# Performance work log

Hardware: AMD Instinct MI355X
Metric: run time of the kernel (lower is better)

Reference implementation:

```python
import jax, jax.numpy as jnp
import numpy as np

N_NODES = 20000
N_EDGES = 320000
N_INPUT = 128
N_HIDDEN = 128
N_LAYERS = 3
N_OUT = 2
C_WEIGHT = 1.0
BN_EPS = 1e-5


def _psi(z):
    # sign(z) * log(1 + |z|), the LorentzNet scalar map
    return jnp.sign(z) * jnp.log1p(jnp.abs(z))


def _mink_dot(a, b):
    # Minkowski inner product, metric diag(+1, -1, ..., -1)
    return a[:, 0] * b[:, 0] - jnp.sum(a[:, 1:] * b[:, 1:], axis=1)


def setup_inputs() -> dict:
    key = jax.random.key(0)
    ks = jax.random.split(key, 12)
    n, h, L = N_INPUT, N_HIDDEN, N_LAYERS
    d_in = 2 * n + 6
    f32 = jnp.float32
    inp = {
        "x": jax.random.normal(ks[0], (N_NODES, n), f32),
        "edge_index": jax.random.randint(ks[1], (2, N_EDGES), 0, N_NODES),
        "edge_attr": jax.random.normal(ks[2], (N_EDGES, 4), f32),
        # phi_e: Linear(d_in->h, no bias), BN(h), ReLU, Linear(h->h), ReLU
        "W1": (jax.random.normal(ks[3], (L, d_in, h), f32) / np.sqrt(d_in)).astype(f32),
        "gamma": jnp.ones((L, h), f32),
        "beta": jnp.zeros((L, h), f32),
        "W2": (jax.random.normal(ks[4], (L, h, h), f32) / np.sqrt(h)).astype(f32),
        "b2": jnp.zeros((L, h), f32),
        # phi_x: Linear(h->h), ReLU, Linear(h->1, no bias, xavier gain 1e-3)
        "Wa": (jax.random.normal(ks[5], (L, h, h), f32) / np.sqrt(h)).astype(f32),
        "ba": jnp.zeros((L, h), f32),
        "Wb": (jax.random.normal(ks[6], (L, h, 1), f32) * 1e-3).astype(f32),
        # phi_m: Linear(h->1), Sigmoid
        "Wm": (jax.random.normal(ks[7], (L, h, 1), f32) / np.sqrt(h)).astype(f32),
        "bm": jnp.zeros((L, 1), f32),
        # final edge_mlp: Linear(h -> N_OUT)
        "We": (jax.random.normal(ks[8], (h, N_OUT), f32) / np.sqrt(h)).astype(f32),
        "be": jnp.zeros((N_OUT,), f32),
    }
    return inp


def _lgeb_layer(x, row, col, edge_attr, W1, gamma, beta, W2, b2, Wa, ba, Wb, Wm, bm):
    x_i = x[row]                       # [E, n] gather (aggregation target)
    x_j = x[col]                       # [E, n]
    x_diff = x_i - x_j                 # [E, n]
    norms = _psi(_mink_dot(x_diff, x_diff))[:, None]   # [E, 1]
    dots = _psi(_mink_dot(x_i, x_j))[:, None]          # [E, 1]
    m = jnp.concatenate([x_i, x_j, edge_attr, norms, dots], axis=1)  # [E, 2n+6]
    # phi_e
    hpre = m @ W1                                       # [E, h]
    mu = jnp.mean(hpre, axis=0)
    var = jnp.mean(jnp.square(hpre - mu), axis=0)       # biased, torch BN train mode
    hbn = (hpre - mu) * jax.lax.rsqrt(var + BN_EPS) * gamma + beta
    hid = jax.nn.relu(hbn)
    m_ij = jax.nn.relu(hid @ W2 + b2)                   # [E, h]
    # phi_m gate
    w = jax.nn.sigmoid(m_ij @ Wm + bm)                  # [E, 1]
    m_ij = m_ij * w
    # phi_x scalar weight on x_diff
    s = jax.nn.relu(m_ij @ Wa + ba) @ Wb                # [E, 1]
    trans = jnp.clip(x_diff * s, -100.0, 100.0)         # [E, n]
    x_agg = jax.ops.segment_sum(trans, row, num_segments=x.shape[0])  # [N, n]
    return x + C_WEIGHT * x_agg


def reference(x, edge_index, edge_attr, W1, gamma, beta, W2, b2,
              Wa, ba, Wb, Wm, bm, We, be):
    row, col = edge_index[0], edge_index[1]
    for l in range(N_LAYERS):
        x = _lgeb_layer(x, row, col, edge_attr,
                        W1[l], gamma[l], beta[l], W2[l], b2[l],
                        Wa[l], ba[l], Wb[l], Wm[l], bm[l])
    return jax.nn.sigmoid(x @ We + be)                  # [N, N_OUT]


if __name__ == "__main__":
    out = reference(**setup_inputs())
    print(out.shape, out.dtype)
```

## Files before the change

### kernel.cpp

```cpp
#include <hip/hip_runtime.h>
#include <math.h>

#define NND 20000
#define NE  320000
#define NF  128
#define EPS 1e-5f
#define TE  64
#define NT  256
#define NTILES (NE / TE)
#define NGRP (NE / 4)
#define EGRID 768
#define XST 136
#define BST 40

typedef short short8 __attribute__((ext_vector_type(8)));
typedef float float4v __attribute__((ext_vector_type(4)));

__device__ __forceinline__ float psif(float z) {
    return copysignf(__logf(1.f + fabsf(z)), z);
}
__device__ __forceinline__ float sigm(float z) {
    return 1.f / (1.f + expf(-z));
}
__device__ __forceinline__ short f2bf(float f) {
    union { float f; unsigned u; } v; v.f = f;
    unsigned r = v.u + 0x7fffu + ((v.u >> 16) & 1u);
    return (short)(r >> 16);
}
__device__ __forceinline__ float bf2f(short u) {
    union { unsigned u; float f; } v; v.u = ((unsigned)(unsigned short)u) << 16;
    return v.f;
}
__device__ __forceinline__ float clipf(float v) {
    return fminf(fmaxf(v, -100.f), 100.f);
}

template<int N>
__device__ __forceinline__ float ror16_add(float v) {
    int r = __builtin_amdgcn_update_dpp(
        0, __float_as_int(v), 0x120 + N , 0xF, 0xF, false);
    return v + __int_as_float(r);
}
__device__ __forceinline__ float rowsum16(float v) {
    v = ror16_add<1>(v);
    v = ror16_add<2>(v);
    v = ror16_add<4>(v);
    v = ror16_add<8>(v);
    return v;
}

__device__ __forceinline__ void stage_b(const unsigned short* __restrict__ wsrc, int wstride,
                                        int ks, short* bt, int t) {
    #pragma unroll
    for (int rr = 0; rr < 2; ++rr) {
        int c = t + rr * 256;
        int n = c >> 2, h = c & 3;
        short8 v = *(const short8*)(wsrc + (size_t)n * wstride + ks * 32 + h * 8);
        *(short8*)(bt + n * BST + h * 8) = v;
    }
}

__device__ __forceinline__ void ldreg_b(const unsigned short* __restrict__ w, int wstride,
                                        int ks, int t, short8* r) {
    #pragma unroll
    for (int rr = 0; rr < 2; ++rr) {
        int c = t + rr * 256;
        int n = c >> 2, h = c & 3;
        r[rr] = *(const short8*)(w + (size_t)n * wstride + ks * 32 + h * 8);
    }
}
__device__ __forceinline__ void wrlds_b(short* bt, int t, const short8* r) {
    #pragma unroll
    for (int rr = 0; rr < 2; ++rr) {
        int c = t + rr * 256;
        int n = c >> 2, h = c & 3;
        *(short8*)(bt + n * BST + h * 8) = r[rr];
    }
}

__global__ __launch_bounds__(NT, 2)
void node_gemm(const float* __restrict__ x,
               const unsigned short* __restrict__ wt,
               float* __restrict__ P,
               unsigned short* __restrict__ rec,
               float* __restrict__ gstats)
{
    __shared__ short lxa[TE * XST];
    __shared__ short lbt[128 * BST];

    const int t = threadIdx.x;
    const int lane = t & 63, quad = lane >> 4, ln15 = lane & 15;
    const int wv = t >> 6, we = wv >> 1, wc = wv & 1;
    const int n0 = blockIdx.x * 64;
    const int ch = blockIdx.y;
    const unsigned short* wsrc = wt + (size_t)ch * 128 * 128;

    if (blockIdx.x == 0 && ch == 0) gstats[t] = 0.f;

    {
        int row = t >> 2, q = t & 3;
        int src = min(n0 + row, NND - 1);
        const float4* xp = (const float4*)(x + (size_t)src * NF) + q * 8;
        #pragma unroll
        for (int u = 0; u < 4; ++u) {
            float4 a = xp[2*u], b = xp[2*u+1];
            short8 s;
            s[0]=f2bf(a.x); s[1]=f2bf(a.y); s[2]=f2bf(a.z); s[3]=f2bf(a.w);
            s[4]=f2bf(b.x); s[5]=f2bf(b.y); s[6]=f2bf(b.z); s[7]=f2bf(b.w);
            *(short8*)(lxa + row * XST + q * 32 + u * 8) = s;
        }
    }

    float4v acc[2][4];
    #pragma unroll
    for (int a = 0; a < 2; ++a)
        #pragma unroll
        for (int b = 0; b < 4; ++b) { float4v z = {0.f,0.f,0.f,0.f}; acc[a][b] = z; }

    for (int ks = 0; ks < 4; ++ks) {
        __syncthreads();
        stage_b(wsrc, NF, ks, lbt, t);
        __syncthreads();
        short8 af[2], bfr[4];
        #pragma unroll
        for (int ef = 0; ef < 2; ++ef)
            af[ef] = *(const short8*)(lxa + (we*32 + ef*16 + ln15) * XST + ks*32 + quad*8);
        #pragma unroll
        for (int fc = 0; fc < 4; ++fc)
            bfr[fc] = *(const short8*)(lbt + (wc*64 + fc*16 + ln15) * BST + quad*8);
        #pragma unroll
        for (int ef = 0; ef < 2; ++ef)
            #pragma unroll
            for (int fc = 0; fc < 4; ++fc)
                acc[ef][fc] = __builtin_amdgcn_mfma_f32_16x16x32_bf16(af[ef], bfr[fc], acc[ef][fc], 0, 0, 0);
    }
    #pragma unroll
    for (int fc = 0; fc < 4; ++fc) {
        int c = wc * 64 + fc * 16 + ln15;
        #pragma unroll
        for (int ef = 0; ef < 2; ++ef)
            #pragma unroll
            for (int rg = 0; rg < 4; ++rg) {
                int nrow = n0 + we * 32 + ef * 16 + quad * 4 + rg;
                if (nrow < NND) {
                    if (ch == 0)
                        P[(size_t)nrow * NF + c] = acc[ef][fc][rg];
                    else
                        rec[(size_t)nrow * 256 + 128 + c] =
                            (unsigned short)f2bf(acc[ef][fc][rg]);
                }
            }
    }
}

__global__ __launch_bounds__(NT)
void pack_x(const float* __restrict__ x, unsigned short* __restrict__ rec)
{
    int i = blockIdx.x * NT + threadIdx.x;
    if (i >= NND * 16) return;
    int n = i >> 4, q = i & 15;
    const float4* xp = (const float4*)(x + (size_t)n * NF + q * 8);
    float4 a = xp[0], b = xp[1];
    short8 s;
    s[0]=f2bf(a.x); s[1]=f2bf(a.y); s[2]=f2bf(a.z); s[3]=f2bf(a.w);
    s[4]=f2bf(b.x); s[5]=f2bf(b.y); s[6]=f2bf(b.z); s[7]=f2bf(b.w);
    *(short8*)(rec + (size_t)n * 256 + q * 8) = s;
}

struct ED { float4 xi0, xi1, pr0, pr1, ea; short8 xj, qj; };

__device__ __forceinline__ void issue_edge(const float* __restrict__ x,
                                           const float* __restrict__ P,
                                           const unsigned short* __restrict__ rec,
                                           const float* __restrict__ eaS,
                                           int e, int2 rc, int c0, ED& d)
{
    const float4* xip = (const float4*)(x + (size_t)rc.x * NF + c0);
    const float4* prp = (const float4*)(P + (size_t)rc.x * NF + c0);
    const short8* rj  = (const short8*)(rec + (size_t)rc.y * 256 + c0);
    d.xi0 = xip[0]; d.xi1 = xip[1];
    d.pr0 = prp[0]; d.pr1 = prp[1];
    d.xj  = rj[0];  d.qj  = rj[16];
    d.ea  = ((const float4*)eaS)[e];
}

__device__ __forceinline__ void compute_edge(const ED& d, int e, int ln15, int c0,
                                             const float (&w6)[6][8],
                                             float (&ss)[8], float (&sq)[8],
                                             unsigned short* __restrict__ hpre)
{
    float xiv[8] = {d.xi0.x, d.xi0.y, d.xi0.z, d.xi0.w,
                    d.xi1.x, d.xi1.y, d.xi1.z, d.xi1.w};
    float nrm = 0.f, dot = 0.f;
    #pragma unroll
    for (int i = 0; i < 8; ++i) {
        float xj = bf2f(d.xj[i]);
        float dd = xiv[i] - xj;
        nrm = fmaf(-dd, dd, nrm);
        dot = fmaf(-xiv[i], xj, dot);
    }
    if (ln15 == 0) {
        float xj0 = bf2f(d.xj[0]);
        float d0 = xiv[0] - xj0;
        nrm += 2.f * d0 * d0;
        dot += 2.f * xiv[0] * xj0;
    }
    nrm = rowsum16(nrm);
    dot = rowsum16(dot);
    const float pn = psif(nrm), pd = psif(dot);

    float prv[8] = {d.pr0.x, d.pr0.y, d.pr0.z, d.pr0.w,
                    d.pr1.x, d.pr1.y, d.pr1.z, d.pr1.w};
    short8 o;
    #pragma unroll
    for (int i = 0; i < 8; ++i) {
        float v = prv[i] + bf2f(d.qj[i]);
        v = fmaf(d.ea.x, w6[0][i], v);
        v = fmaf(d.ea.y, w6[1][i], v);
        v = fmaf(d.ea.z, w6[2][i], v);
        v = fmaf(d.ea.w, w6[3][i], v);
        v = fmaf(pn,     w6[4][i], v);
        v = fmaf(pd,     w6[5][i], v);
        ss[i] += v;
        sq[i] = fmaf(v, v, sq[i]);
        o[i] = f2bf(v);
    }
    *(short8*)(hpre + (size_t)e * NF + c0) = o;
}

__global__ __launch_bounds__(NT, 3)
void edge_pass(const float* __restrict__ x,
               const float* __restrict__ P,
               const unsigned short* __restrict__ rec,
               const int2* __restrict__ rcS,
               const float* __restrict__ eaS,
               const float* __restrict__ W1l,
               unsigned short* __restrict__ hpre,
               float* __restrict__ gstats)
{
    __shared__ float sred[4][256];

    const int t = threadIdx.x;
    const int lane = t & 63;
    const int wv = t >> 6;
    const int gg = lane >> 4;
    const int ln15 = lane & 15;
    const int c0 = ln15 * 8;

    float w6[6][8];
    #pragma unroll
    for (int k = 0; k < 6; ++k) {
        const float4* wp = (const float4*)(W1l + (size_t)(256 + k) * NF + c0);
        float4 a = wp[0], b = wp[1];
        w6[k][0] = a.x; w6[k][1] = a.y; w6[k][2] = a.z; w6[k][3] = a.w;
        w6[k][4] = b.x; w6[k][5] = b.y; w6[k][6] = b.z; w6[k][7] = b.w;
    }

    float ss[8], sq[8];
    #pragma unroll
    for (int i = 0; i < 8; ++i) { ss[i] = 0.f; sq[i] = 0.f; }

    const int wid = blockIdx.x * 4 + wv;
    const int nw  = gridDim.x * 4;
    const int s2  = 2 * nw;

    ED A, B;
    int2 rcA = {0, 0}, rcB = {0, 0}, rcA2 = {0, 0}, rcB2 = {0, 0};
    int gA = wid, gB = wid + nw;

    if (gA < NGRP) {
        rcA = rcS[gA * 4 + gg];
        issue_edge(x, P, rec, eaS, gA * 4 + gg, rcA, c0, A);
    }
    if (gB < NGRP) rcB = rcS[gB * 4 + gg];

    while (gA < NGRP) {
        if (gB < NGRP)
            issue_edge(x, P, rec, eaS, gB * 4 + gg, rcB, c0, B);
        int gA2 = gA + s2;
        if (gA2 < NGRP) rcA2 = rcS[gA2 * 4 + gg];
        compute_edge(A, gA * 4 + gg, ln15, c0, w6, ss, sq, hpre);
        gA = gA2;
        if (gA < NGRP) {
            rcA = rcA2;
            issue_edge(x, P, rec, eaS, gA * 4 + gg, rcA, c0, A);
        }
        int gB2 = gB + s2;
        if (gB2 < NGRP) rcB2 = rcS[gB2 * 4 + gg];
        if (gB < NGRP)
            compute_edge(B, gB * 4 + gg, ln15, c0, w6, ss, sq, hpre);
        gB = gB2; rcB = rcB2;
    }

    #pragma unroll
    for (int i = 0; i < 8; ++i) {
        ss[i] += __shfl_xor(ss[i], 16); ss[i] += __shfl_xor(ss[i], 32);
        sq[i] += __shfl_xor(sq[i], 16); sq[i] += __shfl_xor(sq[i], 32);
    }
    if (lane < 16) {
        #pragma unroll
        for (int i = 0; i < 8; ++i) {
            sred[wv][c0 + i]       = ss[i];
            sred[wv][128 + c0 + i] = sq[i];
        }
    }
    __syncthreads();
    atomicAdd(&gstats[t], sred[0][t] + sred[1][t] + sred[2][t] + sred[3][t]);
}

__global__ __launch_bounds__(NT, 4)
void passB(const unsigned short* __restrict__ hpre,
           const float* __restrict__ gstats,
           const float* __restrict__ gamma,
           const float* __restrict__ beta,
           const unsigned short* __restrict__ wt2,
           const float* __restrict__ b2,
           const unsigned short* __restrict__ wta,
           const float* __restrict__ ba,
           const float* __restrict__ wb,
           const float* __restrict__ wm,
           const float* __restrict__ bm,
           float* __restrict__ sG)
{
    __shared__ short lxi[TE * XST];
    __shared__ short lbt0[128 * BST];
    __shared__ short lbt1[128 * BST];
    __shared__ float gpart[2][TE];
    __shared__ float spart[2][TE];
    __shared__ float wgt[TE];
    __shared__ float scs[NF], sfs[NF];

    const int t = threadIdx.x;
    const int lane = t & 63, quad = lane >> 4, ln15 = lane & 15;
    const int wv = t >> 6, we = wv >> 1, wc = wv & 1;
    const int e0 = blockIdx.x * TE;
    const float bmv = bm[0];

    if (t < NF) {
        float mu  = gstats[t] * (1.f / NE);
        float var = fmaxf(gstats[128 + t] * (1.f / NE) - mu * mu, 0.f);
        float inv = rsqrtf(var + EPS);
        float sc  = gamma[t] * inv;
        scs[t] = sc;
        sfs[t] = beta[t] - mu * sc;
    }
    __syncthreads();

    {
        const int le = t >> 2, q = t & 3;
        const unsigned short* hp = hpre + (size_t)(e0 + le) * NF + q * 32;
        #pragma unroll
        for (int h = 0; h < 4; ++h) {
            short8 v = *(const short8*)(hp + h * 8);
            short o[8];
            #pragma unroll
            for (int i = 0; i < 8; ++i) {
                int chn = q * 32 + h * 8 + i;
                float f = fmaxf(fmaf(bf2f(v[i]), scs[chn], sfs[chn]), 0.f);
                o[i] = f2bf(f);
            }
            *(short8*)(lxi + le * XST + q * 32 + h * 8) = *(short8*)o;
        }
    }

    float4v acc[2][4];
    #pragma unroll
    for (int a = 0; a < 2; ++a)
        #pragma unroll
        for (int b = 0; b < 4; ++b) { float4v z = {0.f,0.f,0.f,0.f}; acc[a][b] = z; }

    {
        short8 pre[2];
        ldreg_b(wt2, NF, 0, t, pre);
        wrlds_b(lbt0, t, pre);
        __syncthreads();
        for (int ks = 0; ks < 4; ++ks) {
            short8 nxt[2];
            if (ks < 3) ldreg_b(wt2, NF, ks + 1, t, nxt);
            const short* cur = (ks & 1) ? lbt1 : lbt0;
            short8 af[2], bfr[4];
            #pragma unroll
            for (int ef = 0; ef < 2; ++ef)
                af[ef] = *(const short8*)(lxi + (we*32 + ef*16 + ln15) * XST + ks*32 + quad*8);
            #pragma unroll
            for (int fc = 0; fc < 4; ++fc)
                bfr[fc] = *(const short8*)(cur + (wc*64 + fc*16 + ln15) * BST + quad*8);
            #pragma unroll
            for (int ef = 0; ef < 2; ++ef)
                #pragma unroll
                for (int fc = 0; fc < 4; ++fc)
                    acc[ef][fc] = __builtin_amdgcn_mfma_f32_16x16x32_bf16(af[ef], bfr[fc], acc[ef][fc], 0, 0, 0);
            if (ks < 3) wrlds_b((ks & 1) ? lbt0 : lbt1, t, nxt);
            __syncthreads();
        }
    }

    {
        float p[2][4] = {{0.f,0.f,0.f,0.f},{0.f,0.f,0.f,0.f}};
        #pragma unroll
        for (int fc = 0; fc < 4; ++fc) {
            int c = wc * 64 + fc * 16 + ln15;
            float bb = b2[c], wmv = wm[c];
            #pragma unroll
            for (int ef = 0; ef < 2; ++ef)
                #pragma unroll
                for (int rg = 0; rg < 4; ++rg) {
                    int r = we * 32 + ef * 16 + quad * 4 + rg;
                    float v = fmaxf(acc[ef][fc][rg] + bb, 0.f);
                    lxi[r * XST + c] = f2bf(v);
                    p[ef][rg] = fmaf(v, wmv, p[ef][rg]);
                }
        }
        #pragma unroll
        for (int ef = 0; ef < 2; ++ef)
            #pragma unroll
            for (int rg = 0; rg < 4; ++rg) {
                p[ef][rg] += __shfl_xor(p[ef][rg], 1);
                p[ef][rg] += __shfl_xor(p[ef][rg], 2);
                p[ef][rg] += __shfl_xor(p[ef][rg], 4);
                p[ef][rg] += __shfl_xor(p[ef][rg], 8);
            }
        if (ln15 == 0) {
            #pragma unroll
            for (int ef = 0; ef < 2; ++ef)
                #pragma unroll
                for (int rg = 0; rg < 4; ++rg)
                    gpart[wc][we * 32 + ef * 16 + quad * 4 + rg] = p[ef][rg];
        }
    }

    #pragma unroll
    for (int a = 0; a < 2; ++a)
        #pragma unroll
        for (int b = 0; b < 4; ++b) { float4v z = {0.f,0.f,0.f,0.f}; acc[a][b] = z; }
    {
        short8 pre[2];
        ldreg_b(wta, NF, 0, t, pre);
        wrlds_b(lbt0, t, pre);
        __syncthreads();
        if (t < TE) wgt[t] = sigm(gpart[0][t] + gpart[1][t] + bmv);
        for (int ks = 0; ks < 4; ++ks) {
            short8 nxt[2];
            if (ks < 3) ldreg_b(wta, NF, ks + 1, t, nxt);
            const short* cur = (ks & 1) ? lbt1 : lbt0;
            short8 af[2], bfr[4];
            #pragma unroll
            for (int ef = 0; ef < 2; ++ef)
                af[ef] = *(const short8*)(lxi + (we*32 + ef*16 + ln15) * XST + ks*32 + quad*8);
            #pragma unroll
            for (int fc = 0; fc < 4; ++fc)
                bfr[fc] = *(const short8*)(cur + (wc*64 + fc*16 + ln15) * BST + quad*8);
            #pragma unroll
            for (int ef = 0; ef < 2; ++ef)
                #pragma unroll
                for (int fc = 0; fc < 4; ++fc)
                    acc[ef][fc] = __builtin_amdgcn_mfma_f32_16x16x32_bf16(af[ef], bfr[fc], acc[ef][fc], 0, 0, 0);
            if (ks < 3) wrlds_b((ks & 1) ? lbt0 : lbt1, t, nxt);
            __syncthreads();
        }
    }
    {
        float p[2][4] = {{0.f,0.f,0.f,0.f},{0.f,0.f,0.f,0.f}};
        #pragma unroll
        for (int fc = 0; fc < 4; ++fc) {
            int c = wc * 64 + fc * 16 + ln15;
            float bav = ba[c], wbv = wb[c];
            #pragma unroll
            for (int ef = 0; ef < 2; ++ef)
                #pragma unroll
                for (int rg = 0; rg < 4; ++rg) {
                    int r = we * 32 + ef * 16 + quad * 4 + rg;
                    float v = fmaxf(fmaf(wgt[r], acc[ef][fc][rg], bav), 0.f);
                    p[ef][rg] = fmaf(v, wbv, p[ef][rg]);
                }
        }
        #pragma unroll
        for (int ef = 0; ef < 2; ++ef)
            #pragma unroll
            for (int rg = 0; rg < 4; ++rg) {
                p[ef][rg] += __shfl_xor(p[ef][rg], 1);
                p[ef][rg] += __shfl_xor(p[ef][rg], 2);
                p[ef][rg] += __shfl_xor(p[ef][rg], 4);
                p[ef][rg] += __shfl_xor(p[ef][rg], 8);
            }
        if (ln15 == 0) {
            #pragma unroll
            for (int ef = 0; ef < 2; ++ef)
                #pragma unroll
                for (int rg = 0; rg < 4; ++rg)
                    spart[wc][we * 32 + ef * 16 + quad * 4 + rg] = p[ef][rg];
        }
    }
    __syncthreads();
    if (t < TE) sG[e0 + t] = spart[0][t] + spart[1][t];
}

__global__ __launch_bounds__(NT)
void hist_k(const int* __restrict__ ei, int* __restrict__ deg)
{
    int e = blockIdx.x * NT + threadIdx.x;
    if (e < NE) atomicAdd(&deg[ei[e]], 1);
}

__global__ __launch_bounds__(NT)
void scan_k(const int* __restrict__ deg, int* __restrict__ rowstart,
            int* __restrict__ cursor)
{
    __shared__ int part[NT];
    const int t = threadIdx.x;
    const int CH = (NND + NT - 1) / NT;
    const int base = t * CH;
    int sum = 0;
    for (int i = 0; i < CH; ++i) {
        int idx = base + i;
        if (idx < NND) sum += deg[idx];
    }
    part[t] = sum;
    __syncthreads();
    int pre = 0;
    for (int j = 0; j < t; ++j) pre += part[j];
    int run = pre;
    for (int i = 0; i < CH; ++i) {
        int idx = base + i;
        if (idx < NND) {
            rowstart[idx] = run;
            cursor[idx]   = run;
            run += deg[idx];
        }
    }
    if (t == NT - 1) rowstart[NND] = run;
}

__global__ __launch_bounds__(NT)
void fill_k(const int* __restrict__ ei, int* __restrict__ cursor,
            int* __restrict__ perm)
{
    int e = blockIdx.x * NT + threadIdx.x;
    if (e < NE) {
        int pos = atomicAdd(&cursor[ei[e]], 1);
        perm[pos] = e;
    }
}

__global__ __launch_bounds__(NT)
void prep_edges(const int* __restrict__ ei, const float* __restrict__ eattr,
                const int* __restrict__ perm,
                int2* __restrict__ rcS, int* __restrict__ colS,
                float* __restrict__ eaS)
{
    int p = blockIdx.x * NT + threadIdx.x;
    if (p >= NE) return;
    int e = perm[p];
    int r = ei[e];
    int c = ei[NE + e];
    rcS[p] = make_int2(r, c);
    colS[p] = c;
    ((float4*)eaS)[p] = ((const float4*)eattr)[e];
}

__global__ __launch_bounds__(NT)
void aggregate_k(const float* __restrict__ x,
                 const float* __restrict__ sG,
                 const int* __restrict__ rowstart,
                 const int* __restrict__ colS,
                 float* __restrict__ xn,
                 unsigned short* __restrict__ rec)
{
    const int w  = (blockIdx.x * NT + threadIdx.x) >> 6;
    const int ln = threadIdx.x & 63;
    if (w >= NND) return;
    const int beg = rowstart[w], end = rowstart[w + 1];
    const float* xr = x + (size_t)w * NF;
    const float xr0 = xr[ln], xr1 = xr[ln + 64];
    float a0 = 0.f, a1 = 0.f;
    int p = beg;
    if (p < end) {
        int c = colS[p];
        float v0 = x[(size_t)c * NF + ln];
        float v1 = x[(size_t)c * NF + 64 + ln];
        for (; p + 1 < end; ++p) {
            int c2 = colS[p + 1];
            float w0 = x[(size_t)c2 * NF + ln];
            float w1 = x[(size_t)c2 * NF + 64 + ln];
            float s = sG[p];
            a0 += clipf((xr0 - v0) * s);
            a1 += clipf((xr1 - v1) * s);
            v0 = w0; v1 = w1;
        }
        float s = sG[p];
        a0 += clipf((xr0 - v0) * s);
        a1 += clipf((xr1 - v1) * s);
    }
    const float o0 = xr0 + a0;
    const float o1 = xr1 + a1;
    xn[(size_t)w * NF + ln]      = o0;
    xn[(size_t)w * NF + ln + 64] = o1;
    rec[(size_t)w * 256 + ln]      = (unsigned short)f2bf(o0);
    rec[(size_t)w * 256 + 64 + ln] = (unsigned short)f2bf(o1);
}

__global__ __launch_bounds__(NT)
void aggregate_final(const float* __restrict__ x,
                     const float* __restrict__ sG,
                     const int* __restrict__ rowstart,
                     const int* __restrict__ colS,
                     const float* __restrict__ We,
                     const float* __restrict__ be,
                     float* __restrict__ out)
{
    const int w  = (blockIdx.x * NT + threadIdx.x) >> 6;
    const int ln = threadIdx.x & 63;
    if (w >= NND) return;
    const int beg = rowstart[w], end = rowstart[w + 1];
    const float* xr = x + (size_t)w * NF;
    const float xr0 = xr[ln], xr1 = xr[ln + 64];
    float a0 = 0.f, a1 = 0.f;
    int p = beg;
    if (p < end) {
        int c = colS[p];
        float v0 = x[(size_t)c * NF + ln];
        float v1 = x[(size_t)c * NF + 64 + ln];
        for (; p + 1 < end; ++p) {
            int c2 = colS[p + 1];
            float w0 = x[(size_t)c2 * NF + ln];
            float w1 = x[(size_t)c2 * NF + 64 + ln];
            float s = sG[p];
            a0 += clipf((xr0 - v0) * s);
            a1 += clipf((xr1 - v1) * s);
            v0 = w0; v1 = w1;
        }
        float s = sG[p];
        a0 += clipf((xr0 - v0) * s);
        a1 += clipf((xr1 - v1) * s);
    }
    const float v0 = xr0 + a0;
    const float v1 = xr1 + a1;
    float o0 = v0 * We[ln * 2]     + v1 * We[(ln + 64) * 2];
    float o1 = v0 * We[ln * 2 + 1] + v1 * We[(ln + 64) * 2 + 1];
    #pragma unroll
    for (int m = 1; m < 64; m <<= 1) { o0 += __shfl_xor(o0, m); o1 += __shfl_xor(o1, m); }
    if (ln == 0) {
        out[w * 2]     = sigm(o0 + be[0]);
        out[w * 2 + 1] = sigm(o1 + be[1]);
    }
}

__global__ __launch_bounds__(NT)
void prep_w1n(const float* __restrict__ W1, unsigned short* __restrict__ wt)
{
    int i = blockIdx.x * NT + threadIdx.x;
    if (i >= 3 * 256 * 128) return;
    int l = i / (256 * 128);
    int r = i % (256 * 128);
    int cc = r / 128, k = r % 128;
    int srow = (cc < 128) ? k : 128 + k;
    int scol = (cc < 128) ? cc : cc - 128;
    wt[i] = (unsigned short)f2bf(W1[((size_t)l * 262 + srow) * 128 + scol]);
}

__global__ __launch_bounds__(NT)
void prep_w128(const float* __restrict__ W, unsigned short* __restrict__ wt)
{
    int i = blockIdx.x * NT + threadIdx.x;
    if (i >= 3 * 128 * 128) return;
    int l = i / (128 * 128);
    int r = i % (128 * 128);
    int n = r / 128, k = r % 128;
    wt[i] = (unsigned short)f2bf(W[((size_t)l * 128 + k) * 128 + n]);
}

extern "C" void kernel_launch(void* const* d_in, const int* in_sizes, int n_in,
                              void* d_out, int out_size, void* d_ws, size_t ws_size,
                              hipStream_t stream) {
    const float* x   = (const float*)d_in[0];
    const int*   ei  = (const int*)d_in[1];
    const float* ea  = (const float*)d_in[2];
    const float* W1  = (const float*)d_in[3];
    const float* ga  = (const float*)d_in[4];
    const float* bet = (const float*)d_in[5];
    const float* W2  = (const float*)d_in[6];
    const float* b2  = (const float*)d_in[7];
    const float* Wa  = (const float*)d_in[8];
    const float* ba  = (const float*)d_in[9];
    const float* Wb  = (const float*)d_in[10];
    const float* Wm  = (const float*)d_in[11];
    const float* bm  = (const float*)d_in[12];
    const float* We  = (const float*)d_in[13];
    const float* be  = (const float*)d_in[14];
    float* out = (float*)d_out;

    char* base = (char*)d_ws;
    size_t off = 0;
    auto alloc = [&](size_t bytes) -> void* {
        off = (off + 31) & ~(size_t)31;
        void* p = base + off;
        off += bytes;
        return p;
    };
    float* gstats   = (float*)alloc(256 * sizeof(float));
    int*   deg      = (int*)alloc(NND * sizeof(int));
    int*   rowstart = (int*)alloc((NND + 1) * sizeof(int));
    int*   cursor   = (int*)alloc(NND * sizeof(int));
    int*   perm     = (int*)alloc(NE * sizeof(int));
    int2*  rcS      = (int2*)alloc((size_t)NE * sizeof(int2));
    int*   colS     = (int*)alloc(NE * sizeof(int));
    float* eaS      = (float*)alloc((size_t)NE * 4 * sizeof(float));
    float* sG       = (float*)alloc(NE * sizeof(float));
    float* xA       = (float*)alloc((size_t)NND * NF * sizeof(float));
    float* xB       = (float*)alloc((size_t)NND * NF * sizeof(float));
    float* P        = (float*)alloc((size_t)NND * NF * sizeof(float));
    unsigned short* rec  = (unsigned short*)alloc((size_t)NND * 256 * 2);
    unsigned short* wt1n = (unsigned short*)alloc((size_t)3 * 256 * 128 * 2);
    unsigned short* wt2  = (unsigned short*)alloc((size_t)3 * 128 * 128 * 2);
    unsigned short* wta  = (unsigned short*)alloc((size_t)3 * 128 * 128 * 2);
    unsigned short* hpreG= (unsigned short*)alloc((size_t)NE * NF * 2);

    prep_w1n <<<(3 * 256 * 128 + NT - 1) / NT, NT, 0, stream>>>(W1, wt1n);
    prep_w128<<<(3 * 128 * 128 + NT - 1) / NT, NT, 0, stream>>>(W2, wt2);
    prep_w128<<<(3 * 128 * 128 + NT - 1) / NT, NT, 0, stream>>>(Wa, wta);

    hipMemsetAsync(deg, 0, NND * sizeof(int), stream);
    hist_k<<<(NE + NT - 1) / NT, NT, 0, stream>>>(ei, deg);
    scan_k<<<1, NT, 0, stream>>>(deg, rowstart, cursor);
    fill_k<<<(NE + NT - 1) / NT, NT, 0, stream>>>(ei, cursor, perm);
    prep_edges<<<(NE + NT - 1) / NT, NT, 0, stream>>>(ei, ea, perm, rcS, colS, eaS);
    pack_x<<<(NND * 16 + NT - 1) / NT, NT, 0, stream>>>(x, rec);

    const float* xc = x;
    float* buf[2] = { xA, xB };

    for (int l = 0; l < 3; ++l) {
        node_gemm<<<dim3((NND + 63) / 64, 2), NT, 0, stream>>>(
            xc, wt1n + (size_t)l * 256 * 128, P, rec, gstats);
        edge_pass<<<EGRID, NT, 0, stream>>>(xc, P, rec, rcS, eaS,
                                            W1 + (size_t)l * 262 * 128, hpreG, gstats);
        passB<<<NTILES, NT, 0, stream>>>(hpreG, gstats, ga + l * NF, bet + l * NF,
                                         wt2 + (size_t)l * 128 * 128, b2 + l * NF,
                                         wta + (size_t)l * 128 * 128, ba + l * NF,
                                         Wb + l * NF, Wm + l * NF, bm + l, sG);
        if (l < 2) {
            float* xn = buf[l & 1];
            aggregate_k<<<(NND * 64 + NT - 1) / NT, NT, 0, stream>>>(xc, sG, rowstart,
                                                                     colS, xn, rec);
            xc = xn;
        } else {
            aggregate_final<<<(NND * 64 + NT - 1) / NT, NT, 0, stream>>>(xc, sG, rowstart,
                                                                         colS, We, be, out);
        }
    }
}
```

Baseline: 655.1 us.

## Load passB weight fragments directly from global into registers, drop LDS staging

In passB the two 128x128 bf16 GEMMs (W2 and Wa) now load their B-operand MFMA fragments straight from global memory into registers, with a one-step register prefetch. This replaces the double-buffered LDS staging and removes the per-k-step __syncthreads barriers and LDS writes. The shuffle-based 16-lane row sums are also replaced by the existing rowsum16 DPP helper. Each wave now fetches its own weight slices from global/L2 instead of sharing them through LDS, and the extra register pressure may affect occupancy at launch bounds of 4.

```diff
diff --git a/kernel.cpp b/kernel.cpp
--- a/kernel.cpp
+++ b/kernel.cpp
@@ -60,22 +60,13 @@
     }
 }
 
-__device__ __forceinline__ void ldreg_b(const unsigned short* __restrict__ w, int wstride,
-                                        int ks, int t, short8* r) {
-    #pragma unroll
-    for (int rr = 0; rr < 2; ++rr) {
-        int c = t + rr * 256;
-        int n = c >> 2, h = c & 3;
-        r[rr] = *(const short8*)(w + (size_t)n * wstride + ks * 32 + h * 8);
-    }
-}
-__device__ __forceinline__ void wrlds_b(short* bt, int t, const short8* r) {
-    #pragma unroll
-    for (int rr = 0; rr < 2; ++rr) {
-        int c = t + rr * 256;
-        int n = c >> 2, h = c & 3;
-        *(short8*)(bt + n * BST + h * 8) = r[rr];
-    }
+__device__ __forceinline__ void ldb_g(const unsigned short* __restrict__ w,
+                                      int ks, int wc, int ln15, int quad,
+                                      short8* bfr) {
+    #pragma unroll
+    for (int fc = 0; fc < 4; ++fc)
+        bfr[fc] = *(const short8*)(w + (size_t)(wc*64 + fc*16 + ln15) * NF
+                                     + ks * 32 + quad * 8);
 }
 
 __global__ __launch_bounds__(NT, 2)
@@ -323,8 +314,6 @@
            float* __restrict__ sG)
 {
     __shared__ short lxi[TE * XST];
-    __shared__ short lbt0[128 * BST];
-    __shared__ short lbt1[128 * BST];
     __shared__ float gpart[2][TE];
     __shared__ float spart[2][TE];
     __shared__ float wgt[TE];
@@ -335,6 +324,9 @@
     const int wv = t >> 6, we = wv >> 1, wc = wv & 1;
     const int e0 = blockIdx.x * TE;
     const float bmv = bm[0];
+
+    short8 bcur[4], bnxt[4];
+    ldb_g(wt2, 0, wc, ln15, quad, bcur);
 
     if (t < NF) {
         float mu  = gstats[t] * (1.f / NE);
@@ -369,31 +361,29 @@
         #pragma unroll
         for (int b = 0; b < 4; ++b) { float4v z = {0.f,0.f,0.f,0.f}; acc[a][b] = z; }
 
-    {
-        short8 pre[2];
-        ldreg_b(wt2, NF, 0, t, pre);
-        wrlds_b(lbt0, t, pre);
-        __syncthreads();
-        for (int ks = 0; ks < 4; ++ks) {
-            short8 nxt[2];
-            if (ks < 3) ldreg_b(wt2, NF, ks + 1, t, nxt);
-            const short* cur = (ks & 1) ? lbt1 : lbt0;
-            short8 af[2], bfr[4];
-            #pragma unroll
-            for (int ef = 0; ef < 2; ++ef)
-                af[ef] = *(const short8*)(lxi + (we*32 + ef*16 + ln15) * XST + ks*32 + quad*8);
+    __syncthreads();
+
+    #pragma unroll
+    for (int ks = 0; ks < 4; ++ks) {
+        if (ks < 3) ldb_g(wt2, ks + 1, wc, ln15, quad, bnxt);
+        short8 af[2];
+        #pragma unroll
+        for (int ef = 0; ef < 2; ++ef)
+            af[ef] = *(const short8*)(lxi + (we*32 + ef*16 + ln15) * XST + ks*32 + quad*8);
+        #pragma unroll
+        for (int ef = 0; ef < 2; ++ef)
             #pragma unroll
             for (int fc = 0; fc < 4; ++fc)
-                bfr[fc] = *(const short8*)(cur + (wc*64 + fc*16 + ln15) * BST + quad*8);
-            #pragma unroll
-            for (int ef = 0; ef < 2; ++ef)
-                #pragma unroll
-                for (int fc = 0; fc < 4; ++fc)
-                    acc[ef][fc] = __builtin_amdgcn_mfma_f32_16x16x32_bf16(af[ef], bfr[fc], acc[ef][fc], 0, 0, 0);
-            if (ks < 3) wrlds_b((ks & 1) ? lbt0 : lbt1, t, nxt);
-            __syncthreads();
-        }
-    }
+                acc[ef][fc] = __builtin_amdgcn_mfma_f32_16x16x32_bf16(af[ef], bcur[fc], acc[ef][fc], 0, 0, 0);
+        if (ks < 3) {
+            bcur[0] = bnxt[0]; bcur[1] = bnxt[1];
+            bcur[2] = bnxt[2]; bcur[3] = bnxt[3];
+        }
+    }
+
+    ldb_g(wta, 0, wc, ln15, quad, bcur);
+
+    __syncthreads();
 
     {
         float p[2][4] = {{0.f,0.f,0.f,0.f},{0.f,0.f,0.f,0.f}};
@@ -414,12 +404,8 @@
         #pragma unroll
         for (int ef = 0; ef < 2; ++ef)
             #pragma unroll
-            for (int rg = 0; rg < 4; ++rg) {
-                p[ef][rg] += __shfl_xor(p[ef][rg], 1);
-                p[ef][rg] += __shfl_xor(p[ef][rg], 2);
-                p[ef][rg] += __shfl_xor(p[ef][rg], 4);
-                p[ef][rg] += __shfl_xor(p[ef][rg], 8);
-            }
+            for (int rg = 0; rg < 4; ++rg)
+                p[ef][rg] = rowsum16(p[ef][rg]);
         if (ln15 == 0) {
             #pragma unroll
             for (int ef = 0; ef < 2; ++ef)
@@ -433,30 +419,26 @@
     for (int a = 0; a < 2; ++a)
         #pragma unroll
         for (int b = 0; b < 4; ++b) { float4v z = {0.f,0.f,0.f,0.f}; acc[a][b] = z; }
-    {
-        short8 pre[2];
-        ldreg_b(wta, NF, 0, t, pre);
-        wrlds_b(lbt0, t, pre);
-        __syncthreads();
-        if (t < TE) wgt[t] = sigm(gpart[0][t] + gpart[1][t] + bmv);
-        for (int ks = 0; ks < 4; ++ks) {
-            short8 nxt[2];
-            if (ks < 3) ldreg_b(wta, NF, ks + 1, t, nxt);
-            const short* cur = (ks & 1) ? lbt1 : lbt0;
-            short8 af[2], bfr[4];
-            #pragma unroll
-            for (int ef = 0; ef < 2; ++ef)
-                af[ef] = *(const short8*)(lxi + (we*32 + ef*16 + ln15) * XST + ks*32 + quad*8);
+
+    __syncthreads();
+
+    if (t < TE) wgt[t] = sigm(gpart[0][t] + gpart[1][t] + bmv);
+
+    #pragma unroll
+    for (int ks = 0; ks < 4; ++ks) {
+        if (ks < 3) ldb_g(wta, ks + 1, wc, ln15, quad, bnxt);
+        short8 af[2];
+        #pragma unroll
+        for (int ef = 0; ef < 2; ++ef)
+            af[ef] = *(const short8*)(lxi + (we*32 + ef*16 + ln15) * XST + ks*32 + quad*8);
+        #pragma unroll
+        for (int ef = 0; ef < 2; ++ef)
             #pragma unroll
             for (int fc = 0; fc < 4; ++fc)
-                bfr[fc] = *(const short8*)(cur + (wc*64 + fc*16 + ln15) * BST + quad*8);
-            #pragma unroll
-            for (int ef = 0; ef < 2; ++ef)
-                #pragma unroll
-                for (int fc = 0; fc < 4; ++fc)
-                    acc[ef][fc] = __builtin_amdgcn_mfma_f32_16x16x32_bf16(af[ef], bfr[fc], acc[ef][fc], 0, 0, 0);
-            if (ks < 3) wrlds_b((ks & 1) ? lbt0 : lbt1, t, nxt);
-            __syncthreads();
+                acc[ef][fc] = __builtin_amdgcn_mfma_f32_16x16x32_bf16(af[ef], bcur[fc], acc[ef][fc], 0, 0, 0);
+        if (ks < 3) {
+            bcur[0] = bnxt[0]; bcur[1] = bnxt[1];
+            bcur[2] = bnxt[2]; bcur[3] = bnxt[3];
         }
     }
     {
@@ -477,12 +459,8 @@
         #pragma unroll
         for (int ef = 0; ef < 2; ++ef)
             #pragma unroll
-            for (int rg = 0; rg < 4; ++rg) {
-                p[ef][rg] += __shfl_xor(p[ef][rg], 1);
-                p[ef][rg] += __shfl_xor(p[ef][rg], 2);
-                p[ef][rg] += __shfl_xor(p[ef][rg], 4);
-                p[ef][rg] += __shfl_xor(p[ef][rg], 8);
-            }
+            for (int rg = 0; rg < 4; ++rg)
+                p[ef][rg] = rowsum16(p[ef][rg]);
         if (ln15 == 0) {
             #pragma unroll
             for (int ef = 0; ef < 2; ++ef)
```

New measurement: 729.3 us. 1.11x slower.
